# Kernel tuning notes

Hardware: AMD Instinct MI355X
Metric: run time of the kernel (lower is better)

The kernel has to match this reference:

```python
import jax, jax.numpy as jnp
import numpy as np
import math

B, S, E, H = 4, 2048, 1024, 1024  # batch, seq, n_embd, head_size


def _rope(q, k, pos):
    # q, k: (B, S, H); pos: (B, S) float
    d = q.shape[-1]
    omega = 1.0 / (10000.0 ** (jnp.arange(d // 2, dtype=jnp.float32) / (d / 2.0)))
    ang = pos[..., None] * omega                      # (B, S, d/2)
    sin = jnp.sin(ang)
    cos = jnp.cos(ang)
    cos_pos = jnp.repeat(cos, 2, axis=-1)             # (B, S, d) [c0,c0,c1,c1,...]
    sin_pos = jnp.repeat(sin, 2, axis=-1)

    def rot(t):
        t_ = jnp.stack([-t[..., 1::2], t[..., 0::2]], axis=-1).reshape(t.shape)
        return t * cos_pos + t_ * sin_pos

    return rot(q), rot(k)


def setup_inputs() -> dict:
    key = jax.random.key(0)
    ks = jax.random.split(key, 9)
    s = 1.0 / math.sqrt(E)
    x = jax.random.normal(ks[0], (B, S, E), dtype=jnp.float32)
    pos = jnp.broadcast_to(jnp.arange(S, dtype=jnp.float32), (B, S))
    mask = jnp.triu(jnp.ones((S, S), dtype=bool), k=1)  # causal: True = masked out
    Wq = jax.random.normal(ks[1], (H, E), dtype=jnp.float32) * s
    Wk = jax.random.normal(ks[2], (H, E), dtype=jnp.float32) * s
    Wv = jax.random.normal(ks[3], (H, E), dtype=jnp.float32) * s
    bq = jax.random.normal(ks[4], (H,), dtype=jnp.float32) * 0.01
    bk = jax.random.normal(ks[5], (H,), dtype=jnp.float32) * 0.01
    bv = jax.random.normal(ks[6], (H,), dtype=jnp.float32) * 0.01
    Wo = jax.random.normal(ks[7], (H, H), dtype=jnp.float32) * (1.0 / math.sqrt(H))
    bo = jax.random.normal(ks[8], (H,), dtype=jnp.float32) * 0.01
    return {"x": x, "pos": pos, "mask": mask, "Wq": Wq, "bq": bq,
            "Wk": Wk, "bk": bk, "Wv": Wv, "bv": bv, "Wo": Wo, "bo": bo}


def reference(x, pos, mask, Wq, bq, Wk, bk, Wv, bv, Wo, bo):
    n_embd = x.shape[-1]
    q = jnp.einsum('bse,he->bsh', x, Wq) + bq
    k = jnp.einsum('bse,he->bsh', x, Wk) + bk
    v = jnp.einsum('bse,he->bsh', x, Wv) + bv
    q, k = _rope(q, k, pos)
    # NOTE: original divides by sqrt(x.shape[-1]) == sqrt(n_embd), not sqrt(head_size)
    w = jnp.einsum('bqh,bkh->bqk', q, k) / jnp.sqrt(jnp.float32(n_embd))
    w = jnp.where(mask, jnp.float32(-1e7), w)
    w = jax.nn.softmax(w, axis=-1)  # dropout is identity in eval mode
    out = jnp.einsum('bqk,bkh->bqh', w, v)
    out = jnp.einsum('bsh,oh->bso', out, Wo) + bo
    return out
```

## Files before the change

### kernel.cpp

```cpp
#include <hip/hip_runtime.h>
#include <hip/hip_bf16.h>
#include <stdint.h>

typedef __attribute__((ext_vector_type(4))) float  f32x4;
typedef __attribute__((ext_vector_type(8))) short  short8;
typedef __attribute__((ext_vector_type(8))) __bf16 bf16x8;

#define GLB_AS __attribute__((address_space(1)))
#define LDS_AS __attribute__((address_space(3)))

__device__ __forceinline__ float bf2f(ushort u) {
    union { uint u32; float f; } c; c.u32 = (uint)u << 16; return c.f;
}
__device__ __forceinline__ ushort f2bf(float f) {
    union { float f; uint u32; } c; c.f = f;
    uint x = c.u32;
    return (ushort)((x + 0x7fffu + ((x >> 16) & 1u)) >> 16);
}

__device__ __forceinline__ void storeC(float* p, float v)  { *p = v; }
__device__ __forceinline__ void storeC(ushort* p, float v) { *p = f2bf(v); }

template<int N> __device__ __forceinline__ void vmwait() {
    if constexpr (N == 0) asm volatile("s_waitcnt vmcnt(0)" ::: "memory");
    else if constexpr (N == 2) asm volatile("s_waitcnt vmcnt(2)" ::: "memory");
    else if constexpr (N == 4) asm volatile("s_waitcnt vmcnt(4)" ::: "memory");
}

__global__ __launch_bounds__(256) void convert_f32_bf16(
    const float* __restrict__ in, ushort* __restrict__ out, long n)
{
    long i0 = ((long)blockIdx.x * 256 + threadIdx.x) * 8;
    long stride = (long)gridDim.x * 256 * 8;
    for (long i = i0; i < n; i += stride) {
        float4 a = *(const float4*)(in + i);
        float4 b = *(const float4*)(in + i + 4);
        short8 o;
        o[0] = (short)f2bf(a.x); o[1] = (short)f2bf(a.y);
        o[2] = (short)f2bf(a.z); o[3] = (short)f2bf(a.w);
        o[4] = (short)f2bf(b.x); o[5] = (short)f2bf(b.y);
        o[6] = (short)f2bf(b.z); o[7] = (short)f2bf(b.w);
        *(short8*)(out + i) = o;
    }
}

__global__ __launch_bounds__(256) void rope_inplace(
    ushort* __restrict__ qk, const float* __restrict__ pos)
{
    const int row = blockIdx.x;
    const float p = pos[row];
    const size_t base = (size_t)row * 2048;
    const int tid = threadIdx.x;
#pragma unroll
    for (int t = 0; t < 2; ++t) {
        int j = tid + t * 256;
        float omega = exp2f(-(float)j * (13.287712379549449f / 512.0f));
        float ang = p * omega;
        float sn, cs;
        sincosf(ang, &sn, &cs);
        uint pq = *(uint*)(qk + base + 2 * j);
        float q0 = bf2f((ushort)(pq & 0xffff)), q1 = bf2f((ushort)(pq >> 16));
        float r0 = q0 * cs - q1 * sn, r1 = q1 * cs + q0 * sn;
        *(uint*)(qk + base + 2 * j) = (uint)f2bf(r0) | ((uint)f2bf(r1) << 16);
        uint pk = *(uint*)(qk + base + 1024 + 2 * j);
        float k0 = bf2f((ushort)(pk & 0xffff)), k1 = bf2f((ushort)(pk >> 16));
        float s0 = k0 * cs - k1 * sn, s1 = k1 * cs + k0 * sn;
        *(uint*)(qk + base + 1024 + 2 * j) = (uint)f2bf(s0) | ((uint)f2bf(s1) << 16);
    }
}

__global__ __launch_bounds__(256) void softmax_rows(ushort* __restrict__ P)
{
    const size_t base = (size_t)blockIdx.x * 2048;
    const int tid = threadIdx.x;
    const int lane = tid & 63, wid = tid >> 6;
    short8 v = *(const short8*)(P + base + tid * 8);
    float f[8];
#pragma unroll
    for (int j = 0; j < 8; ++j) f[j] = bf2f((ushort)v[j]);
    float mx = f[0];
#pragma unroll
    for (int j = 1; j < 8; ++j) mx = fmaxf(mx, f[j]);
#pragma unroll
    for (int o = 32; o; o >>= 1) mx = fmaxf(mx, __shfl_xor(mx, o, 64));
    __shared__ float redm[4], reds[4];
    if (lane == 0) redm[wid] = mx;
    __syncthreads();
    mx = fmaxf(fmaxf(redm[0], redm[1]), fmaxf(redm[2], redm[3]));
    float s = 0.f;
#pragma unroll
    for (int j = 0; j < 8; ++j) { f[j] = __expf(f[j] - mx); s += f[j]; }
#pragma unroll
    for (int o = 32; o; o >>= 1) s += __shfl_xor(s, o, 64);
    if (lane == 0) reds[wid] = s;
    __syncthreads();
    s = reds[0] + reds[1] + reds[2] + reds[3];
    float inv = 1.0f / s;
    short8 o8;
#pragma unroll
    for (int j = 0; j < 8; ++j) o8[j] = (short)f2bf(f[j] * inv);
    *(short8*)(P + base + tid * 8) = o8;
}


template<int C, int H>
__device__ __forceinline__ void stageT(ushort (&L)[2][2][8192],
    const ushort* __restrict__ G, int tileBase, int ld, int t,
    int wid, int sr, int scS)
{
#pragma unroll
    for (int i = 0; i < 2; ++i) {
        const int row = (wid * 2 + i) * 8 + sr;
        const ushort* g = G + (size_t)(tileBase + H * 128 + row) * ld + t * 64 + scS * 8;
        __builtin_amdgcn_global_load_lds((const GLB_AS void*)g,
            (LDS_AS void*)(&L[C][H][(wid * 2 + i) * 512]), 16, 0, 0);
    }
}

template<int C, int H>
__device__ __forceinline__ void readA(const ushort (&As)[2][2][8192],
    short8 (&afr)[4][2], int wr, int fr, int kg)
{
#pragma unroll
    for (int m = 0; m < 4; ++m) {
        const int r = wr * 64 + m * 16 + fr;
        const int sw = ((r >> 2) & 1) << 4;
#pragma unroll
        for (int kk = 0; kk < 2; ++kk)
            afr[m][kk] = *(const short8*)&As[C][H][r * 64 + ((kk * 32 + kg * 8) ^ sw)];
    }
}

template<int C, int H>
__device__ __forceinline__ void readB(const ushort (&Bs)[2][2][8192],
    short8 (&bfr)[2][2], int wc, int fr, int kg)
{
#pragma unroll
    for (int n = 0; n < 2; ++n) {
        const int r = wc * 32 + n * 16 + fr;
        const int sw = ((r >> 2) & 1) << 4;
#pragma unroll
        for (int kk = 0; kk < 2; ++kk)
            bfr[n][kk] = *(const short8*)&Bs[C][H][r * 64 + ((kk * 32 + kg * 8) ^ sw)];
    }
}

template<int MQ, int NQ>
__device__ __forceinline__ void domfma(f32x4 (&acc)[2][2][4][2],
    const short8 (&afr)[4][2], const short8 (&bfr)[2][2])
{
#pragma unroll
    for (int kk = 0; kk < 2; ++kk)
#pragma unroll
        for (int m = 0; m < 4; ++m)
#pragma unroll
            for (int n = 0; n < 2; ++n)
                acc[MQ][NQ][m][n] = __builtin_amdgcn_mfma_f32_16x16x32_bf16(
                    __builtin_bit_cast(bf16x8, afr[m][kk]),
                    __builtin_bit_cast(bf16x8, bfr[n][kk]),
                    acc[MQ][NQ][m][n], 0, 0, 0);
}

#define PHASE_MID() \
    __builtin_amdgcn_s_barrier(); \
    asm volatile("s_waitcnt lgkmcnt(0)" ::: "memory"); \
    __builtin_amdgcn_s_setprio(1)
#define PHASE_END(VM) \
    __builtin_amdgcn_s_setprio(0); \
    vmwait<VM>(); \
    __builtin_amdgcn_s_barrier()

template<int C, bool LAST>
__device__ __forceinline__ void tile_body(
    ushort (&As)[2][2][8192], ushort (&Bs)[2][2][8192],
    f32x4 (&acc)[2][2][4][2],
    const ushort* __restrict__ A, const ushort* __restrict__ B,
    int rowBase, int colBase, int lda, int ldb, int tNext,
    int wid, int wr, int wc, int fr, int kg, int sr, int scS)
{
    short8 afr[4][2], bfr[2][2];
    readA<C, 0>(As, afr, wr, fr, kg);
    readB<C, 0>(Bs, bfr, wc, fr, kg);
    if constexpr (!LAST) stageT<C ^ 1, 0>(Bs, B, colBase, ldb, tNext, wid, sr, scS);
    PHASE_MID();
    domfma<0, 0>(acc, afr, bfr);
    PHASE_END((LAST ? 2 : 4));
    readA<C, 1>(As, afr, wr, fr, kg);
    if constexpr (!LAST) stageT<C ^ 1, 0>(As, A, rowBase, lda, tNext, wid, sr, scS);
    PHASE_MID();
    domfma<1, 0>(acc, afr, bfr);
    PHASE_END((LAST ? 0 : 4));
    readB<C, 1>(Bs, bfr, wc, fr, kg);
    if constexpr (!LAST) stageT<C ^ 1, 1>(As, A, rowBase, lda, tNext, wid, sr, scS);
    PHASE_MID();
    domfma<1, 1>(acc, afr, bfr);
    PHASE_END((LAST ? 0 : 4));
    readA<C, 0>(As, afr, wr, fr, kg);
    if constexpr (!LAST) stageT<C ^ 1, 1>(Bs, B, colBase, ldb, tNext, wid, sr, scS);
    PHASE_MID();
    domfma<0, 1>(acc, afr, bfr);
    PHASE_END((LAST ? 0 : 4));
}

template<bool BIAS_COL, bool BIAS_ROW, bool CAUSAL_MASK, bool CAUSAL_K, typename OutT>
__global__ __launch_bounds__(512, 2) void gemm256(
    const ushort* __restrict__ A, const ushort* __restrict__ B,
    OutT* __restrict__ C, const float* __restrict__ bias,
    int K, int lda, int ldb, int ldc,
    long sA, long sB, long sC, float scale)
{
    __shared__ ushort As[2][2][8192];
    __shared__ ushort Bs[2][2][8192];
    A += (long)blockIdx.z * sA;
    B += (long)blockIdx.z * sB;
    C += (long)blockIdx.z * sC;
    const int tid = threadIdx.x;
    const int lane = tid & 63;
    const int wid = tid >> 6;
    const int wr = wid >> 2, wc = wid & 3;
    const int rowBase = blockIdx.y * 256;
    const int colBase = blockIdx.x * 256;
    const int fr = lane & 15;
    const int kg = lane >> 4;

    f32x4 acc[2][2][4][2] = {};

    const bool skip = CAUSAL_MASK && (colBase > rowBase + 255);
    int Kend = K;
    if (CAUSAL_K) { int ke = rowBase + 256; Kend = ke < K ? ke : K; }

    if (!skip) {
        const int sr = lane >> 3;
        const int scS = (lane & 7) ^ (((lane >> 5) & 1) << 1);
        stageT<0, 0>(Bs, B, colBase, ldb, 0, wid, sr, scS);
        stageT<0, 0>(As, A, rowBase, lda, 0, wid, sr, scS);
        stageT<0, 1>(As, A, rowBase, lda, 0, wid, sr, scS);
        stageT<0, 1>(Bs, B, colBase, ldb, 0, wid, sr, scS);
        vmwait<0>();
        __builtin_amdgcn_s_barrier();

        const int NT = Kend >> 6;
        int t = 0;
        for (; t + 2 < NT; t += 2) {
            tile_body<0, false>(As, Bs, acc, A, B, rowBase, colBase, lda, ldb, t + 1,
                                wid, wr, wc, fr, kg, sr, scS);
            tile_body<1, false>(As, Bs, acc, A, B, rowBase, colBase, lda, ldb, t + 2,
                                wid, wr, wc, fr, kg, sr, scS);
        }
        tile_body<0, false>(As, Bs, acc, A, B, rowBase, colBase, lda, ldb, t + 1,
                            wid, wr, wc, fr, kg, sr, scS);
        tile_body<1, true>(As, Bs, acc, A, B, rowBase, colBase, lda, ldb, 0,
                           wid, wr, wc, fr, kg, sr, scS);
    }

#pragma unroll
    for (int mq = 0; mq < 2; ++mq)
#pragma unroll
        for (int nq = 0; nq < 2; ++nq)
#pragma unroll
            for (int m = 0; m < 4; ++m)
#pragma unroll
                for (int n = 0; n < 2; ++n)
#pragma unroll
                    for (int j = 0; j < 4; ++j) {
                        int row = rowBase + mq * 128 + wr * 64 + m * 16 + kg * 4 + j;
                        int col = colBase + nq * 128 + wc * 32 + n * 16 + fr;
                        float v = acc[mq][nq][m][n][j] * scale;
                        if (BIAS_COL) v += bias[col];
                        if (BIAS_ROW) v += bias[row];
                        if (CAUSAL_MASK && (col > row)) v = -1e7f;
                        storeC(C + (size_t)row * ldc + col, v);
                    }
}

extern "C" void kernel_launch(void* const* d_in, const int* in_sizes, int n_in,
                              void* d_out, int out_size, void* d_ws, size_t ws_size,
                              hipStream_t stream)
{
    const float* x   = (const float*)d_in[0];
    const float* pos = (const float*)d_in[1];
    const float* Wq = (const float*)d_in[3]; const float* bq = (const float*)d_in[4];
    const float* Wk = (const float*)d_in[5]; const float* bk = (const float*)d_in[6];
    const float* Wv = (const float*)d_in[7]; const float* bv = (const float*)d_in[8];
    const float* Wo = (const float*)d_in[9]; const float* bo = (const float*)d_in[10];
    float* out = (float*)d_out;

    const int S = 2048, E = 1024, H = 1024, Bz = 4;
    const int Mtot = Bz * S;

    ushort* xb   = (ushort*)d_ws;
    ushort* wqkb = xb   + (size_t)Mtot * E;
    ushort* wvb  = wqkb + (size_t)2 * H * E;
    ushort* wob  = wvb  + (size_t)H * E;
    ushort* qk   = wob  + (size_t)H * H;
    ushort* vt   = qk   + (size_t)Mtot * 2 * H;
    ushort* P    = vt   + (size_t)H * Mtot;
    float*  bqk  = (float*)(P + (size_t)Bz * S * S);
    ushort* O    = xb;

    convert_f32_bf16<<<2048, 256, 0, stream>>>(x,  xb,   (long)Mtot * E);
    convert_f32_bf16<<<512,  256, 0, stream>>>(Wq, wqkb, (long)H * E);
    convert_f32_bf16<<<512,  256, 0, stream>>>(Wk, wqkb + (size_t)H * E, (long)H * E);
    convert_f32_bf16<<<512,  256, 0, stream>>>(Wv, wvb,  (long)H * E);
    convert_f32_bf16<<<512,  256, 0, stream>>>(Wo, wob,  (long)H * H);
    hipMemcpyAsync(bqk,     bq, H * sizeof(float), hipMemcpyDeviceToDevice, stream);
    hipMemcpyAsync(bqk + H, bk, H * sizeof(float), hipMemcpyDeviceToDevice, stream);

    gemm256<true, false, false, false, ushort><<<dim3(8, 32, 1), 512, 0, stream>>>(
        xb, wqkb, qk, bqk, E, E, E, 2 * H, 0, 0, 0, 1.0f);
    gemm256<false, true, false, false, ushort><<<dim3(32, 4, 1), 512, 0, stream>>>(
        wvb, xb, vt, bv, E, E, E, Mtot, 0, 0, 0, 1.0f);

    rope_inplace<<<Mtot, 256, 0, stream>>>(qk, pos);

    gemm256<false, false, true, false, ushort><<<dim3(8, 8, Bz), 512, 0, stream>>>(
        qk, qk + H, P, nullptr, H, 2 * H, 2 * H, S,
        (long)S * 2 * H, (long)S * 2 * H, (long)S * S, 0.03125f);

    softmax_rows<<<Mtot, 256, 0, stream>>>(P);

    gemm256<false, false, false, true, ushort><<<dim3(4, 8, Bz), 512, 0, stream>>>(
        P, vt, O, nullptr, S, S, Mtot, H,
        (long)S * S, (long)S, (long)S * H, 1.0f);

    gemm256<true, false, false, false, float><<<dim3(4, 32, 1), 512, 0, stream>>>(
        O, wob, out, bo, H, H, H, H, 0, 0, 0, 1.0f);
}
```

Measured before the change: 403.3 us.

## Deepen GEMM prefetch pipeline, change LDS swizzle, and remap workgroups across XCDs

Restructures the 256x256 GEMM main loop so the next K-tile's halves are prefetched further ahead, including part of tile t+2 into the current buffer. Vmcnt waits are consolidated to one per group instead of one per phase. The LDS XOR swizzle becomes a full 8-way row-based pattern to cut bank conflicts. A flat workgroup-ID remap spreads consecutive blocks across the 8 XCDs for better L2 locality. The risks are a harder-to-verify pipeline with buffer-reuse hazards, and a swizzle that assumes the grid size divides by 8.

```diff
diff --git a/kernel.cpp b/kernel.cpp
--- a/kernel.cpp
+++ b/kernel.cpp
@@ -23,8 +23,7 @@
 
 template<int N> __device__ __forceinline__ void vmwait() {
     if constexpr (N == 0) asm volatile("s_waitcnt vmcnt(0)" ::: "memory");
-    else if constexpr (N == 2) asm volatile("s_waitcnt vmcnt(2)" ::: "memory");
-    else if constexpr (N == 4) asm volatile("s_waitcnt vmcnt(4)" ::: "memory");
+    else if constexpr (N == 6) asm volatile("s_waitcnt vmcnt(6)" ::: "memory");
 }
 
 __global__ __launch_bounds__(256) void convert_f32_bf16(
@@ -103,45 +102,46 @@
 }
 
 
-template<int C, int H>
+template<int BUF, int HALF>
 __device__ __forceinline__ void stageT(ushort (&L)[2][2][8192],
-    const ushort* __restrict__ G, int tileBase, int ld, int t,
+    const ushort* __restrict__ G, int tileBase, int ld, int tk,
     int wid, int sr, int scS)
 {
 #pragma unroll
     for (int i = 0; i < 2; ++i) {
-        const int row = (wid * 2 + i) * 8 + sr;
-        const ushort* g = G + (size_t)(tileBase + H * 128 + row) * ld + t * 64 + scS * 8;
+        const int chunk = wid * 2 + i;
+        const ushort* g = G + (size_t)(tileBase + HALF * 128 + chunk * 8 + sr) * ld
+                        + tk * 64 + scS * 8;
         __builtin_amdgcn_global_load_lds((const GLB_AS void*)g,
-            (LDS_AS void*)(&L[C][H][(wid * 2 + i) * 512]), 16, 0, 0);
-    }
-}
-
-template<int C, int H>
+            (LDS_AS void*)(&L[BUF][HALF][chunk * 512]), 16, 0, 0);
+    }
+}
+
+template<int BUF, int HALF>
 __device__ __forceinline__ void readA(const ushort (&As)[2][2][8192],
     short8 (&afr)[4][2], int wr, int fr, int kg)
 {
+    const int sw = (fr & 7) << 3;
 #pragma unroll
     for (int m = 0; m < 4; ++m) {
         const int r = wr * 64 + m * 16 + fr;
-        const int sw = ((r >> 2) & 1) << 4;
 #pragma unroll
         for (int kk = 0; kk < 2; ++kk)
-            afr[m][kk] = *(const short8*)&As[C][H][r * 64 + ((kk * 32 + kg * 8) ^ sw)];
-    }
-}
-
-template<int C, int H>
+            afr[m][kk] = *(const short8*)&As[BUF][HALF][r * 64 + ((kk * 32 + kg * 8) ^ sw)];
+    }
+}
+
+template<int BUF, int HALF>
 __device__ __forceinline__ void readB(const ushort (&Bs)[2][2][8192],
     short8 (&bfr)[2][2], int wc, int fr, int kg)
 {
+    const int sw = (fr & 7) << 3;
 #pragma unroll
     for (int n = 0; n < 2; ++n) {
         const int r = wc * 32 + n * 16 + fr;
-        const int sw = ((r >> 2) & 1) << 4;
 #pragma unroll
         for (int kk = 0; kk < 2; ++kk)
-            bfr[n][kk] = *(const short8*)&Bs[C][H][r * 64 + ((kk * 32 + kg * 8) ^ sw)];
+            bfr[n][kk] = *(const short8*)&Bs[BUF][HALF][r * 64 + ((kk * 32 + kg * 8) ^ sw)];
     }
 }
 
@@ -164,42 +164,46 @@
 #define PHASE_MID() \
     __builtin_amdgcn_s_barrier(); \
     asm volatile("s_waitcnt lgkmcnt(0)" ::: "memory"); \
+    __builtin_amdgcn_sched_barrier(0); \
     __builtin_amdgcn_s_setprio(1)
-#define PHASE_END(VM) \
+#define PHASE_END() \
     __builtin_amdgcn_s_setprio(0); \
-    vmwait<VM>(); \
     __builtin_amdgcn_s_barrier()
 
-template<int C, bool LAST>
-__device__ __forceinline__ void tile_body(
+template<int BUF, int MODE>
+__device__ __forceinline__ void group(
     ushort (&As)[2][2][8192], ushort (&Bs)[2][2][8192],
     f32x4 (&acc)[2][2][4][2],
     const ushort* __restrict__ A, const ushort* __restrict__ B,
-    int rowBase, int colBase, int lda, int ldb, int tNext,
+    int rowBase, int colBase, int lda, int ldb, int t,
     int wid, int wr, int wc, int fr, int kg, int sr, int scS)
 {
     short8 afr[4][2], bfr[2][2];
-    readA<C, 0>(As, afr, wr, fr, kg);
-    readB<C, 0>(Bs, bfr, wc, fr, kg);
-    if constexpr (!LAST) stageT<C ^ 1, 0>(Bs, B, colBase, ldb, tNext, wid, sr, scS);
+    readA<BUF, 0>(As, afr, wr, fr, kg);
+    readB<BUF, 0>(Bs, bfr, wc, fr, kg);
+    if constexpr (MODE != 2) stageT<BUF ^ 1, 0>(As, A, rowBase, lda, t + 1, wid, sr, scS);
+    asm volatile("s_waitcnt lgkmcnt(8)" ::: "memory");
     PHASE_MID();
     domfma<0, 0>(acc, afr, bfr);
-    PHASE_END((LAST ? 2 : 4));
-    readA<C, 1>(As, afr, wr, fr, kg);
-    if constexpr (!LAST) stageT<C ^ 1, 0>(As, A, rowBase, lda, tNext, wid, sr, scS);
+    PHASE_END();
+    readA<BUF, 1>(As, afr, wr, fr, kg);
+    if constexpr (MODE == 0) stageT<BUF, 0>(Bs, B, colBase, ldb, t + 2, wid, sr, scS);
     PHASE_MID();
     domfma<1, 0>(acc, afr, bfr);
-    PHASE_END((LAST ? 0 : 4));
-    readB<C, 1>(Bs, bfr, wc, fr, kg);
-    if constexpr (!LAST) stageT<C ^ 1, 1>(As, A, rowBase, lda, tNext, wid, sr, scS);
+    PHASE_END();
+    readB<BUF, 1>(Bs, bfr, wc, fr, kg);
+    if constexpr (MODE == 0) stageT<BUF, 1>(As, A, rowBase, lda, t + 2, wid, sr, scS);
     PHASE_MID();
     domfma<1, 1>(acc, afr, bfr);
-    PHASE_END((LAST ? 0 : 4));
-    readA<C, 0>(As, afr, wr, fr, kg);
-    if constexpr (!LAST) stageT<C ^ 1, 1>(Bs, B, colBase, ldb, tNext, wid, sr, scS);
+    PHASE_END();
+    readA<BUF, 0>(As, afr, wr, fr, kg);
+    if constexpr (MODE == 0) stageT<BUF, 1>(Bs, B, colBase, ldb, t + 2, wid, sr, scS);
     PHASE_MID();
     domfma<0, 1>(acc, afr, bfr);
-    PHASE_END((LAST ? 0 : 4));
+    __builtin_amdgcn_s_setprio(0);
+    if constexpr (MODE == 0) vmwait<6>();
+    else if constexpr (MODE == 1) vmwait<0>();
+    __builtin_amdgcn_s_barrier();
 }
 
 template<bool BIAS_COL, bool BIAS_ROW, bool CAUSAL_MASK, bool CAUSAL_K, typename OutT>
@@ -211,15 +215,26 @@
 {
     __shared__ ushort As[2][2][8192];
     __shared__ ushort Bs[2][2][8192];
-    A += (long)blockIdx.z * sA;
-    B += (long)blockIdx.z * sB;
-    C += (long)blockIdx.z * sC;
+
+    const int nx = gridDim.x, ny = gridDim.y;
+    int flat = blockIdx.x + nx * (blockIdx.y + ny * blockIdx.z);
+    const int nwg = nx * ny * gridDim.z;
+    const int qq = nwg >> 3;
+    int swz = (flat & 7) * qq + (flat >> 3);
+    const int bx = swz % nx;
+    int rest = swz / nx;
+    const int by = rest % ny;
+    const int bz = rest / ny;
+
+    A += (long)bz * sA;
+    B += (long)bz * sB;
+    C += (long)bz * sC;
     const int tid = threadIdx.x;
     const int lane = tid & 63;
     const int wid = tid >> 6;
     const int wr = wid >> 2, wc = wid & 3;
-    const int rowBase = blockIdx.y * 256;
-    const int colBase = blockIdx.x * 256;
+    const int rowBase = by * 256;
+    const int colBase = bx * 256;
     const int fr = lane & 15;
     const int kg = lane >> 4;
 
@@ -231,26 +246,29 @@
 
     if (!skip) {
         const int sr = lane >> 3;
-        const int scS = (lane & 7) ^ (((lane >> 5) & 1) << 1);
+        const int scS = (lane & 7) ^ (lane >> 3);
+        stageT<0, 0>(As, A, rowBase, lda, 0, wid, sr, scS);
         stageT<0, 0>(Bs, B, colBase, ldb, 0, wid, sr, scS);
-        stageT<0, 0>(As, A, rowBase, lda, 0, wid, sr, scS);
         stageT<0, 1>(As, A, rowBase, lda, 0, wid, sr, scS);
         stageT<0, 1>(Bs, B, colBase, ldb, 0, wid, sr, scS);
-        vmwait<0>();
+        stageT<1, 0>(Bs, B, colBase, ldb, 1, wid, sr, scS);
+        stageT<1, 1>(As, A, rowBase, lda, 1, wid, sr, scS);
+        stageT<1, 1>(Bs, B, colBase, ldb, 1, wid, sr, scS);
+        vmwait<6>();
         __builtin_amdgcn_s_barrier();
 
         const int NT = Kend >> 6;
         int t = 0;
-        for (; t + 2 < NT; t += 2) {
-            tile_body<0, false>(As, Bs, acc, A, B, rowBase, colBase, lda, ldb, t + 1,
-                                wid, wr, wc, fr, kg, sr, scS);
-            tile_body<1, false>(As, Bs, acc, A, B, rowBase, colBase, lda, ldb, t + 2,
-                                wid, wr, wc, fr, kg, sr, scS);
+        for (; t + 3 < NT; t += 2) {
+            group<0, 0>(As, Bs, acc, A, B, rowBase, colBase, lda, ldb, t,
+                        wid, wr, wc, fr, kg, sr, scS);
+            group<1, 0>(As, Bs, acc, A, B, rowBase, colBase, lda, ldb, t + 1,
+                        wid, wr, wc, fr, kg, sr, scS);
         }
-        tile_body<0, false>(As, Bs, acc, A, B, rowBase, colBase, lda, ldb, t + 1,
-                            wid, wr, wc, fr, kg, sr, scS);
-        tile_body<1, true>(As, Bs, acc, A, B, rowBase, colBase, lda, ldb, 0,
-                           wid, wr, wc, fr, kg, sr, scS);
+        group<0, 1>(As, Bs, acc, A, B, rowBase, colBase, lda, ldb, t,
+                    wid, wr, wc, fr, kg, sr, scS);
+        group<1, 2>(As, Bs, acc, A, B, rowBase, colBase, lda, ldb, t + 1,
+                    wid, wr, wc, fr, kg, sr, scS);
     }
 
 #pragma unroll
```

New measurement: 382.5 us. 1.05x faster.
